# Optimization experiments

Measured on AMD Instinct MI355X. Metric: run time of the kernel, lower is better.

## Reference

```python
import jax, jax.numpy as jnp
import numpy as np

N_NODES = 65536   # entity nodes across batched docs
N_EDGES = 32768   # edges per etype
D_CTX = 768       # PTM hidden size ('n' feature)
D_REL = 97        # relation_num (out_feature)
CHUNK = 1024      # edge chunk for the per-edge bilinear


def setup_inputs() -> dict:
    key = jax.random.key(0)
    ks = jax.random.split(key, 10)
    n = jax.random.normal(ks[0], (N_NODES, D_CTX), jnp.float32)
    e_inter = jax.random.normal(ks[1], (N_EDGES, D_REL), jnp.float32)
    e_intra = jax.random.normal(ks[2], (N_EDGES, D_REL), jnp.float32)
    # nn.Bilinear(768, 97, 1, bias=False): weight [1, 768, 97]
    W_bl = jax.random.normal(ks[3], (1, D_CTX, D_REL), jnp.float32) * 0.02
    # nn.Bilinear(194, 194, 97): weight [97, 194, 194], bias [97]
    W_bl1 = jax.random.normal(ks[4], (D_REL, 2 * D_REL, 2 * D_REL), jnp.float32) * 0.02
    b_bl1 = jnp.zeros((D_REL,), jnp.float32)
    src_inter = jax.random.randint(ks[5], (N_EDGES,), 0, N_NODES, jnp.int32)
    dst_inter = jax.random.randint(ks[6], (N_EDGES,), 0, N_NODES, jnp.int32)
    src_intra = jax.random.randint(ks[7], (N_EDGES,), 0, N_NODES, jnp.int32)
    dst_intra = jax.random.randint(ks[8], (N_EDGES,), 0, N_NODES, jnp.int32)
    return {"n": n, "e_inter": e_inter, "e_intra": e_intra,
            "W_bl": W_bl, "W_bl1": W_bl1, "b_bl1": b_bl1,
            "src_inter": src_inter, "dst_inter": dst_inter,
            "src_intra": src_intra, "dst_intra": dst_intra}


def reference(n, e_inter, e_intra, W_bl, W_bl1, b_bl1,
              src_inter, dst_inter, src_intra, dst_intra):
    num_nodes = n.shape[0]
    # node_reduce: score = bilinear(n[dst], e) -> softmax over incoming edges
    # bl(src_n, e) = n[dst] @ W_bl[0] @ e  (precompute node projection once)
    proj = n @ W_bl[0]                                  # [N, D_REL]

    def node_reduce(e, dst):
        s = jnp.sum(proj[dst] * e, axis=-1)             # per-edge score [E]
        smax = jax.ops.segment_max(s, dst, num_segments=num_nodes)
        ex = jnp.exp(s - smax[dst])
        denom = jax.ops.segment_sum(ex, dst, num_segments=num_nodes)
        alpha = ex / denom[dst]                          # segment softmax
        # attention-weighted sum of mailbox messages -> [N, D_REL]
        return jax.ops.segment_sum(e * alpha[:, None], dst, num_segments=num_nodes)

    # multi_update_all(..., 'stack') over etypes ['inter','intra'] then flatten
    rel = jnp.concatenate([node_reduce(e_inter, dst_inter),
                           node_reduce(e_intra, dst_intra)], axis=-1)  # [N, 194]

    def edge_gate(e, src, dst):
        s_rel = rel[src]                                 # [E, 194]
        d_rel = rel[dst]                                 # [E, 194]
        d_in = s_rel.shape[1]

        def f(args):
            s, d = args                                  # [CHUNK, 194]
            return jnp.einsum('ei,kij,ej->ek', s, W_bl1, d, optimize=True) + b_bl1

        gate = jax.lax.map(f, (s_rel.reshape(-1, CHUNK, d_in),
                               d_rel.reshape(-1, CHUNK, d_in)))
        gate = gate.reshape(e.shape[0], -1)              # [E, D_REL]
        return e + jax.nn.sigmoid(gate) * e

    out_inter = edge_gate(e_inter, src_inter, dst_inter)
    out_intra = edge_gate(e_intra, src_intra, dst_intra)
    return jnp.stack([out_inter, out_intra])             # [2, E, D_REL]
```

## Files before the change

kernel.cpp:

```cpp
#include <hip/hip_runtime.h>
#include <hip/hip_bf16.h>
#include <stdint.h>


typedef __attribute__((ext_vector_type(8))) short short8;
typedef __attribute__((ext_vector_type(4))) float f32x4;
typedef _Float16 half8 __attribute__((ext_vector_type(8)));

#define NN 65536
#define NE1 32768
#define NEG 65536
#define DC 768
#define DR 97
#define DR2 194
#define RELSTR 200
#define KI 194
#define KS 7
#define NT 7
#define EPB 128
#define SSTR 200
#define DSTR 232
#define PSTR 72
#define NDESC_G 2176

#define OFF_REL   0ull
#define OFF_BPK   52428800ull
#define OFF_IDX   62164992ull
#define OFF_SMAX  62427136ull
#define OFF_DEN   62951424ull
#define OFF_META  63475712ull
#define OFF_DESC  63475968ull
#define OFF_WPK   63510784ull

static __device__ __forceinline__ unsigned fkey(float f) {
    unsigned b = __float_as_uint(f);
    return (b & 0x80000000u) ? ~b : (b | 0x80000000u);
}
static __device__ __forceinline__ float funkey(unsigned k) {
    return __uint_as_float((k & 0x80000000u) ? (k & 0x7fffffffu) : ~k);
}
static __device__ __forceinline__ unsigned pk2(_Float16 a, _Float16 b) {
    union { _Float16 h[2]; unsigned u; } x;
    x.h[0] = a; x.h[1] = b;
    return x.u;
}
static __device__ __forceinline__ int nstate(bool zi, bool zx) {
    return zi ? (zx ? 3 : 2) : (zx ? 1 : 0);
}
static __device__ __forceinline__ int nsplit_of(int b) {
    return (b == 0) ? 7 : ((b == 1 || b == 2) ? 4 : 2);
}
static __device__ __forceinline__ int kindbase_of(int b) {
    const int kb[9] = {0, 9, 15, 7, 13, 19, 7, 13, 19};
    return kb[b];
}

__global__ void build_bpk(const float* __restrict__ W, half8* __restrict__ Bpk) {
    int id = blockIdx.x * blockDim.x + threadIdx.x;
    const int total = KI * KS * NT * 64;
    if (id >= total) return;
    int l = id & 63;
    int g = id >> 6;
    int t = g % NT;
    int ks = (g / NT) % KS;
    int i = g / (NT * KS);
    int kk = t * 16 + (l & 15);
    int jb = ks * 32 + (l >> 4) * 8;
    half8 pk;
#pragma unroll
    for (int m = 0; m < 8; ++m) {
        int j = jb + m;
        float f = (kk < DR && j < DR2) ? W[(size_t)kk * (DR2 * DR2) + i * DR2 + j] : 0.f;
        pk[m] = (_Float16)f;
    }
    Bpk[id] = pk;
}

__global__ void build_wpk(const float* __restrict__ Wb, half8* __restrict__ Wpk) {
    int id = blockIdx.x * blockDim.x + threadIdx.x;
    const int total = 24 * NT * 64;
    if (id >= total) return;
    int l = id & 63;
    int g = id >> 6;
    int t = g % NT;
    int k2 = g / NT;
    int col = t * 16 + (l & 15);
    int j0 = k2 * 32 + (l >> 4) * 8;
    half8 pk;
#pragma unroll
    for (int m = 0; m < 8; ++m) {
        float f = (col < DR) ? Wb[(size_t)(j0 + m) * DR + col] : 0.f;
        pk[m] = (_Float16)f;
    }
    Wpk[id] = pk;
}

__launch_bounds__(512, 8)
__global__ void proj_mfma(const float* __restrict__ nmat, const half8* __restrict__ Wpk,
                          float* __restrict__ proj) {
    __shared__ __align__(16) _Float16 a_lds[128][PSTR];
    int tid = threadIdx.x;
    int r0 = blockIdx.x << 7;
    int w = tid >> 6, lane = tid & 63;
    int er = (w << 4) + (lane & 15);
    int lk = lane >> 4;

    f32x4 acc[NT];
#pragma unroll
    for (int t = 0; t < NT; ++t) acc[t] = (f32x4){0.f, 0.f, 0.f, 0.f};

    int srow = tid >> 2;
    int sc0 = (tid & 3) << 4;
    const float* nrow = nmat + (size_t)(r0 + srow) * DC + sc0;

    for (int k0 = 0; k0 < DC; k0 += 64) {
        __syncthreads();
        {
            const f32x4* p = (const f32x4*)(nrow + k0);
            _Float16* dst = &a_lds[srow][sc0];
#pragma unroll
            for (int q = 0; q < 4; ++q) {
                f32x4 v = p[q];
                *(unsigned*)&dst[q * 4]     = pk2((_Float16)v[0], (_Float16)v[1]);
                *(unsigned*)&dst[q * 4 + 2] = pk2((_Float16)v[2], (_Float16)v[3]);
            }
        }
        __syncthreads();
#pragma unroll
        for (int kk = 0; kk < 2; ++kk) {
            half8 af = *(const half8*)&a_lds[er][kk * 32 + lk * 8];
            const half8* bp = Wpk + (size_t)((k0 >> 5) + kk) * (NT * 64) + lane;
#pragma unroll
            for (int t = 0; t < NT; ++t)
                acc[t] = __builtin_amdgcn_mfma_f32_16x16x32_f16(af, bp[t * 64], acc[t], 0, 0, 0);
        }
    }

#pragma unroll
    for (int t = 0; t < NT; ++t) {
        int col = t * 16 + (lane & 15);
        if (col < DR) {
#pragma unroll
            for (int r = 0; r < 4; ++r) {
                int row = r0 + (w << 4) + lk * 4 + r;
                proj[(size_t)row * DR + col] = acc[t][r];
            }
        }
    }
}

__global__ void score_kernel(const float* __restrict__ proj,
                             const float* __restrict__ e_inter, const float* __restrict__ e_intra,
                             const int* __restrict__ dst_inter, const int* __restrict__ dst_intra,
                             float* __restrict__ s_buf, unsigned* __restrict__ smax_key) {
    int wid = (blockIdx.x * blockDim.x + threadIdx.x) >> 6;
    int lane = threadIdx.x & 63;
    if (wid >= NEG) return;
    int et = wid >> 15, le = wid & (NE1 - 1);
    const float* e = (et ? e_intra : e_inter) + (size_t)le * DR;
    int dst = (et ? dst_intra : dst_inter)[le];
    const float* pr = proj + (size_t)dst * DR;
    float p = pr[lane] * e[lane];
    if (lane < DR - 64) p += pr[lane + 64] * e[lane + 64];
#pragma unroll
    for (int off = 32; off > 0; off >>= 1) p += __shfl_down(p, off);
    if (lane == 0) {
        s_buf[wid] = p;
        atomicMax(&smax_key[et * NN + dst], fkey(p));
    }
}

__global__ void accum_kernel(const float* __restrict__ s_buf,
                             const float* __restrict__ e_inter, const float* __restrict__ e_intra,
                             const int* __restrict__ dst_inter, const int* __restrict__ dst_intra,
                             const unsigned* __restrict__ smax_key,
                             float* __restrict__ denom, float* __restrict__ rel) {
    int wid = (blockIdx.x * blockDim.x + threadIdx.x) >> 6;
    int lane = threadIdx.x & 63;
    if (wid >= NEG) return;
    int et = wid >> 15, le = wid & (NE1 - 1);
    const float* e = (et ? e_intra : e_inter) + (size_t)le * DR;
    int dst = (et ? dst_intra : dst_inter)[le];
    float s = s_buf[wid];
    float mx = funkey(smax_key[et * NN + dst]);
    float ex = __expf(s - mx);
    if (lane == 0) atomicAdd(&denom[et * NN + dst], ex);
    float* rrow = rel + (size_t)dst * RELSTR + et * DR;
    atomicAdd(&rrow[lane], e[lane] * ex);
    if (lane < DR - 64) atomicAdd(&rrow[lane + 64], e[lane + 64] * ex);
}

__global__ void dinv_kernel(float* __restrict__ denom) {
    int i = blockIdx.x * blockDim.x + threadIdx.x;
    if (i < 2 * NN) {
        float d = denom[i];
        denom[i] = (d > 0.f) ? (1.f / d) : 0.f;
    }
}

__global__ void classify_kernel(const float* __restrict__ dinv,
                                const int* __restrict__ src_inter, const int* __restrict__ dst_inter,
                                const int* __restrict__ src_intra, const int* __restrict__ dst_intra,
                                unsigned* __restrict__ meta) {
    __shared__ unsigned h[16];
    if (threadIdx.x < 16) h[threadIdx.x] = 0;
    __syncthreads();
    int gid = blockIdx.x * blockDim.x + threadIdx.x;
    if (gid < NEG) {
        int et = gid >> 15, le = gid & (NE1 - 1);
        int sn = (et ? src_intra : src_inter)[le];
        int dn = (et ? dst_intra : dst_inter)[le];
        int ss = nstate(dinv[sn] == 0.f, dinv[NN + sn] == 0.f);
        int ds = nstate(dinv[dn] == 0.f, dinv[NN + dn] == 0.f);
        int b = (ss == 3 || ds == 3) ? 9 : ss * 3 + ds;
        atomicAdd(&h[b], 1u);
    }
    __syncthreads();
    if (threadIdx.x < 10 && h[threadIdx.x])
        atomicAdd(&meta[threadIdx.x], h[threadIdx.x]);
}

__global__ void setup1_kernel(unsigned* __restrict__ meta) {
    if (threadIdx.x != 0 || blockIdx.x != 0) return;
    unsigned run = 0;
    for (int b = 0; b < 10; ++b) {
        meta[32 + b] = run;
        meta[16 + b] = run;
        run += meta[b];
    }
    unsigned c = 0;
    for (int b = 0; b < 9; ++b) {
        meta[52 + b] = c;
        c += ((meta[b] + EPB - 1) / EPB) * (unsigned)nsplit_of(b);
    }
    meta[48] = c;
}

__global__ void setup2_kernel(const unsigned* __restrict__ meta, uint4* __restrict__ desc) {
    int j = blockIdx.x * blockDim.x + threadIdx.x;
    if (j >= (int)meta[48]) return;
    int b = 8;
    for (int q = 1; q < 9; ++q)
        if (j < (int)meta[52 + q]) { b = q - 1; break; }
    int p = j - (int)meta[52 + b];
    int ns = nsplit_of(b);
    int ci = p / ns;
    int si = p - ci * ns;
    int cnt = (int)meta[b];
    int cbase = (int)meta[32 + b] + ci * EPB;
    int ccnt = cnt - ci * EPB;
    if (ccnt > EPB) ccnt = EPB;
    int kind = kindbase_of(b) + si;
    int sclass = b / 3;
    desc[j] = make_uint4((unsigned)kind, (unsigned)cbase, (unsigned)ccnt, (unsigned)sclass);
}

__global__ void scatter_kernel(const float* __restrict__ dinv,
                               const int* __restrict__ src_inter, const int* __restrict__ dst_inter,
                               const int* __restrict__ src_intra, const int* __restrict__ dst_intra,
                               unsigned* __restrict__ meta, int* __restrict__ idxbuf) {
    __shared__ unsigned cur[16];
    __shared__ unsigned base[16];
    if (threadIdx.x < 16) cur[threadIdx.x] = 0;
    __syncthreads();
    int gid = blockIdx.x * blockDim.x + threadIdx.x;
    int b = -1;
    unsigned r = 0;
    if (gid < NEG) {
        int et = gid >> 15, le = gid & (NE1 - 1);
        int sn = (et ? src_intra : src_inter)[le];
        int dn = (et ? dst_intra : dst_inter)[le];
        int ss = nstate(dinv[sn] == 0.f, dinv[NN + sn] == 0.f);
        int ds = nstate(dinv[dn] == 0.f, dinv[NN + dn] == 0.f);
        b = (ss == 3 || ds == 3) ? 9 : ss * 3 + ds;
        r = atomicAdd(&cur[b], 1u);
    }
    __syncthreads();
    if (threadIdx.x < 10 && cur[threadIdx.x])
        base[threadIdx.x] = atomicAdd(&meta[16 + threadIdx.x], cur[threadIdx.x]);
    __syncthreads();
    if (b >= 0) idxbuf[base[b] + r] = gid;
}

__global__ void skip_kernel(const unsigned* __restrict__ meta, const int* __restrict__ idxbuf,
                            const float* __restrict__ e_inter, const float* __restrict__ e_intra,
                            const float* __restrict__ bias, float* __restrict__ out) {
    int n9 = (int)meta[9];
    int base9 = (int)meta[41];
    int k = threadIdx.x;
    float g = 0.f;
    if (k < DR) {
        float b = bias[k];
        g = 1.f + 1.f / (1.f + __expf(-b));
    }
    for (int q = blockIdx.x; q < n9; q += gridDim.x) {
        int gid = idxbuf[base9 + q];
        int et = gid >> 15, le = gid & (NE1 - 1);
        const float* e = (et ? e_intra : e_inter) + (size_t)le * DR;
        if (k < DR) out[(size_t)gid * DR + k] = e[k] * g;
    }
}

#define GATE_BODY(KS0v, KS1v, T0v, T1v)                                        \
    {                                                                          \
        constexpr int NKSv = (KS1v) - (KS0v);                                  \
        constexpr int NTTv = (T1v) - (T0v);                                    \
        f32x4 acc[NTTv];                                                       \
        _Pragma("unroll")                                                      \
        for (int tt = 0; tt < NTTv; ++tt) acc[tt] = (f32x4){0.f, 0.f, 0.f, 0.f}; \
        const half8* bl = Bpk + lane;                                          \
        for (int i = i0; i < iEnd; ++i) {                                      \
            _Float16 sa = buf[er * SSTR + i];                                  \
            half8 sv = {sa, sa, sa, sa, sa, sa, sa, sa};                       \
            const half8* bi = bl + (size_t)((i * KS + (KS0v)) * NT + (T0v)) * 64; \
            _Pragma("unroll")                                                  \
            for (int ks = 0; ks < NKSv; ++ks) {                                \
                half8 af = sv * dv[(KS0v) + ks];                               \
                _Pragma("unroll")                                              \
                for (int tt = 0; tt < NTTv; ++tt) {                            \
                    half8 bv = bi[(ks * NT + tt) * 64];                        \
                    acc[tt] = __builtin_amdgcn_mfma_f32_16x16x32_f16(af, bv, acc[tt], 0, 0, 0); \
                }                                                              \
            }                                                                  \
        }                                                                      \
        _Pragma("unroll")                                                      \
        for (int r = 0; r < 4; ++r) {                                          \
            int row = (w << 4) + lk * 4 + r;                                   \
            if (row < ccnt) {                                                  \
                int gid = idxbuf[cbase + row];                                 \
                int et = gid >> 15, le = gid & (NE1 - 1);                      \
                const float* e = (et ? e_intra : e_inter) + (size_t)le * DR;   \
                float* o = out + (size_t)gid * DR;                             \
                _Pragma("unroll")                                              \
                for (int tt = 0; tt < NTTv; ++tt) {                            \
                    int k = ((T0v) + tt) * 16 + (lane & 15);                   \
                    if (k < DR) {                                              \
                        float g = acc[tt][r] + bias[k];                        \
                        float sg = 1.f / (1.f + __expf(-g));                   \
                        o[k] = e[k] * (1.f + sg);                              \
                    }                                                          \
                }                                                              \
            }                                                                  \
        }                                                                      \
    }

__launch_bounds__(512, 1)
__global__ void gate_all(const float* __restrict__ rel, const float* __restrict__ dinv,
                         const half8* __restrict__ Bpk, const float* __restrict__ bias,
                         const int* __restrict__ src_inter, const int* __restrict__ dst_inter,
                         const int* __restrict__ src_intra, const int* __restrict__ dst_intra,
                         const float* __restrict__ e_inter, const float* __restrict__ e_intra,
                         const int* __restrict__ idxbuf, const unsigned* __restrict__ meta,
                         const uint4* __restrict__ desc, float* __restrict__ out) {
    if (blockIdx.x >= meta[48]) return;
    uint4 de = desc[blockIdx.x];
    int kind = (int)de.x;
    int cbase = (int)de.y;
    int ccnt = (int)de.z;
    int sclass = (int)de.w;
    int i0 = (sclass == 2) ? DR : 0;
    int iEnd = (sclass == 0) ? DR2 : (i0 + DR);

    __shared__ __align__(16) _Float16 buf[EPB * DSTR];
    int tid = threadIdx.x;
    int w = tid >> 6;
    int lane = tid & 63;
    int lk = lane >> 4;
    int er = (w << 4) + (lane & 15);

    if (tid < 256) {
        int edge = tid >> 1;
        int h = tid & 1;
        int rc = cbase + ((edge < ccnt) ? edge : (ccnt - 1));
        int gid = idxbuf[rc];
        int et = gid >> 15, le = gid & (NE1 - 1);
        int dn = (et ? dst_intra : dst_inter)[le];
        float di0 = dinv[dn];
        float di1 = dinv[NN + dn];
        const f32x4* rp = (const f32x4*)(rel + (size_t)dn * RELSTR + h * 100);
        _Float16* row = &buf[edge * DSTR];
#pragma unroll
        for (int q = 0; q < 25; ++q) {
            f32x4 v = rp[q];
            int c = h * 100 + q * 4;
            _Float16 h0 = (_Float16)(v[0] * ((c + 0 < DR) ? di0 : di1));
            _Float16 h1 = (_Float16)(v[1] * ((c + 1 < DR) ? di0 : di1));
            _Float16 h2 = (_Float16)(v[2] * ((c + 2 < DR) ? di0 : di1));
            _Float16 h3 = (_Float16)(v[3] * ((c + 3 < DR) ? di0 : di1));
            *(unsigned*)&row[c] = pk2(h0, h1);
            *(unsigned*)&row[c + 2] = pk2(h2, h3);
        }
        if (h) {
            short8 z = (short8)(short)0;
#pragma unroll
            for (int q = 0; q < 3; ++q)
                *(short8*)&row[200 + q * 8] = z;
        }
    }
    __syncthreads();

    half8 dv[KS];
#pragma unroll
    for (int ks = 0; ks < KS; ++ks)
        dv[ks] = *(const half8*)&buf[er * DSTR + ks * 32 + lk * 8];
    __syncthreads();

    if (tid < 256) {
        int edge = tid >> 1;
        int h = tid & 1;
        int rc = cbase + ((edge < ccnt) ? edge : (ccnt - 1));
        int gid = idxbuf[rc];
        int et = gid >> 15, le = gid & (NE1 - 1);
        int sn = (et ? src_intra : src_inter)[le];
        float di0 = dinv[sn];
        float di1 = dinv[NN + sn];
        const f32x4* rp = (const f32x4*)(rel + (size_t)sn * RELSTR + h * 100);
        _Float16* row = &buf[edge * SSTR];
#pragma unroll
        for (int q = 0; q < 25; ++q) {
            f32x4 v = rp[q];
            int c = h * 100 + q * 4;
            _Float16 h0 = (_Float16)(v[0] * ((c + 0 < DR) ? di0 : di1));
            _Float16 h1 = (_Float16)(v[1] * ((c + 1 < DR) ? di0 : di1));
            _Float16 h2 = (_Float16)(v[2] * ((c + 2 < DR) ? di0 : di1));
            _Float16 h3 = (_Float16)(v[3] * ((c + 3 < DR) ? di0 : di1));
            *(unsigned*)&row[c] = pk2(h0, h1);
            *(unsigned*)&row[c + 2] = pk2(h2, h3);
        }
    }
    __syncthreads();

    switch (kind) {
        case 0:  GATE_BODY(0, 7, 0, 1); break;
        case 1:  GATE_BODY(0, 7, 1, 2); break;
        case 2:  GATE_BODY(0, 7, 2, 3); break;
        case 3:  GATE_BODY(0, 7, 3, 4); break;
        case 4:  GATE_BODY(0, 7, 4, 5); break;
        case 5:  GATE_BODY(0, 7, 5, 6); break;
        case 6:  GATE_BODY(0, 7, 6, 7); break;
        case 7:  GATE_BODY(0, 7, 0, 4); break;
        case 8:  GATE_BODY(0, 7, 4, 7); break;
        case 9:  GATE_BODY(0, 4, 0, 2); break;
        case 10: GATE_BODY(0, 4, 2, 4); break;
        case 11: GATE_BODY(0, 4, 4, 6); break;
        case 12: GATE_BODY(0, 4, 6, 7); break;
        case 13: GATE_BODY(0, 4, 0, 4); break;
        case 14: GATE_BODY(0, 4, 4, 7); break;
        case 15: GATE_BODY(3, 7, 0, 2); break;
        case 16: GATE_BODY(3, 7, 2, 4); break;
        case 17: GATE_BODY(3, 7, 4, 6); break;
        case 18: GATE_BODY(3, 7, 6, 7); break;
        case 19: GATE_BODY(3, 7, 0, 4); break;
        case 20: GATE_BODY(3, 7, 4, 7); break;
        default: break;
    }
}

extern "C" void kernel_launch(void* const* d_in, const int* in_sizes, int n_in,
                              void* d_out, int out_size, void* d_ws, size_t ws_size,
                              hipStream_t stream) {
    (void)in_sizes; (void)n_in; (void)out_size; (void)ws_size;
    const float* nmat     = (const float*)d_in[0];
    const float* e_inter  = (const float*)d_in[1];
    const float* e_intra  = (const float*)d_in[2];
    const float* W_bl     = (const float*)d_in[3];
    const float* W_bl1    = (const float*)d_in[4];
    const float* b_bl1    = (const float*)d_in[5];
    const int* src_inter  = (const int*)d_in[6];
    const int* dst_inter  = (const int*)d_in[7];
    const int* src_intra  = (const int*)d_in[8];
    const int* dst_intra  = (const int*)d_in[9];
    float* out = (float*)d_out;

    char* ws = (char*)d_ws;
    float* regA     = (float*)(ws + OFF_REL);
    half8* Bpk      = (half8*)(ws + OFF_BPK);
    int* idxbuf     = (int*)(ws + OFF_IDX);
    float* s_buf    = (float*)(ws + OFF_IDX);
    unsigned* smax  = (unsigned*)(ws + OFF_SMAX);
    float* denom    = (float*)(ws + OFF_DEN);
    unsigned* meta  = (unsigned*)(ws + OFF_META);
    uint4* desc     = (uint4*)(ws + OFF_DESC);
    half8* Wpk      = (half8*)(ws + OFF_WPK);

    hipMemsetAsync(smax, 0, 524288, stream);
    hipMemsetAsync(denom, 0, 524288, stream);
    hipMemsetAsync(meta, 0, 256, stream);

    build_bpk<<<(KI * KS * NT * 64 + 255) / 256, 256, 0, stream>>>(W_bl1, Bpk);
    build_wpk<<<(24 * NT * 64 + 255) / 256, 256, 0, stream>>>(W_bl, Wpk);
    proj_mfma<<<NN / 128, 512, 0, stream>>>(nmat, Wpk, regA);
    score_kernel<<<NEG / 4, 256, 0, stream>>>(regA, e_inter, e_intra, dst_inter, dst_intra,
                                              s_buf, smax);
    hipMemsetAsync(regA, 0, 52428800, stream);
    accum_kernel<<<NEG / 4, 256, 0, stream>>>(s_buf, e_inter, e_intra, dst_inter, dst_intra,
                                              smax, denom, regA);
    dinv_kernel<<<512, 256, 0, stream>>>(denom);
    classify_kernel<<<NEG / 256, 256, 0, stream>>>(denom, src_inter, dst_inter,
                                                   src_intra, dst_intra, meta);
    setup1_kernel<<<1, 64, 0, stream>>>(meta);
    setup2_kernel<<<(NDESC_G + 255) / 256, 256, 0, stream>>>(meta, desc);
    scatter_kernel<<<NEG / 256, 256, 0, stream>>>(denom, src_inter, dst_inter,
                                                  src_intra, dst_intra, meta, idxbuf);
    skip_kernel<<<2048, 128, 0, stream>>>(meta, idxbuf, e_inter, e_intra, b_bl1, out);
    gate_all<<<NDESC_G, 512, 0, stream>>>(regA, denom, Bpk, b_bl1,
                                          src_inter, dst_inter, src_intra, dst_intra,
                                          e_inter, e_intra, idxbuf, meta, desc, out);
}
```

Before: 644.0 us.

## Process two 16-edge row tiles per wave in gate kernel to reuse B fragments

Each wave in the gate kernel now computes two 16-edge MFMA tiles with separate accumulators, so every B-fragment load from the packed bilinear weight feeds two MFMAs. Blocks shrink from 512 to 256 threads, with launch bounds allowing three blocks per CU. The padded dst buffer stride is replaced by masking the tail K fragment in registers. The aim is to halve global weight traffic per MFMA and raise occupancy, at the cost of roughly doubled accumulator and dv register use.

```diff
diff --git a/kernel.cpp b/kernel.cpp
--- a/kernel.cpp
+++ b/kernel.cpp
@@ -19,7 +19,6 @@
 #define NT 7
 #define EPB 128
 #define SSTR 200
-#define DSTR 232
 #define PSTR 72
 #define NDESC_G 2176
 
@@ -305,27 +304,34 @@
     {                                                                          \
         constexpr int NKSv = (KS1v) - (KS0v);                                  \
         constexpr int NTTv = (T1v) - (T0v);                                    \
-        f32x4 acc[NTTv];                                                       \
+        f32x4 acc0[NTTv], acc1[NTTv];                                          \
         _Pragma("unroll")                                                      \
-        for (int tt = 0; tt < NTTv; ++tt) acc[tt] = (f32x4){0.f, 0.f, 0.f, 0.f}; \
+        for (int tt = 0; tt < NTTv; ++tt) {                                    \
+            acc0[tt] = (f32x4){0.f, 0.f, 0.f, 0.f};                            \
+            acc1[tt] = (f32x4){0.f, 0.f, 0.f, 0.f};                            \
+        }                                                                      \
         const half8* bl = Bpk + lane;                                          \
         for (int i = i0; i < iEnd; ++i) {                                      \
-            _Float16 sa = buf[er * SSTR + i];                                  \
-            half8 sv = {sa, sa, sa, sa, sa, sa, sa, sa};                       \
+            _Float16 s0 = buf[er0 * SSTR + i];                                 \
+            _Float16 s1 = buf[er1 * SSTR + i];                                 \
+            half8 sv0 = {s0, s0, s0, s0, s0, s0, s0, s0};                      \
+            half8 sv1 = {s1, s1, s1, s1, s1, s1, s1, s1};                      \
             const half8* bi = bl + (size_t)((i * KS + (KS0v)) * NT + (T0v)) * 64; \
             _Pragma("unroll")                                                  \
             for (int ks = 0; ks < NKSv; ++ks) {                                \
-                half8 af = sv * dv[(KS0v) + ks];                               \
+                half8 af0 = sv0 * dv0[(KS0v) + ks];                            \
+                half8 af1 = sv1 * dv1[(KS0v) + ks];                            \
                 _Pragma("unroll")                                              \
                 for (int tt = 0; tt < NTTv; ++tt) {                            \
                     half8 bv = bi[(ks * NT + tt) * 64];                        \
-                    acc[tt] = __builtin_amdgcn_mfma_f32_16x16x32_f16(af, bv, acc[tt], 0, 0, 0); \
+                    acc0[tt] = __builtin_amdgcn_mfma_f32_16x16x32_f16(af0, bv, acc0[tt], 0, 0, 0); \
+                    acc1[tt] = __builtin_amdgcn_mfma_f32_16x16x32_f16(af1, bv, acc1[tt], 0, 0, 0); \
                 }                                                              \
             }                                                                  \
         }                                                                      \
         _Pragma("unroll")                                                      \
         for (int r = 0; r < 4; ++r) {                                          \
-            int row = (w << 4) + lk * 4 + r;                                   \
+            int row = (w << 5) + lk * 4 + r;                                   \
             if (row < ccnt) {                                                  \
                 int gid = idxbuf[cbase + row];                                 \
                 int et = gid >> 15, le = gid & (NE1 - 1);                      \
@@ -335,16 +341,35 @@
                 for (int tt = 0; tt < NTTv; ++tt) {                            \
                     int k = ((T0v) + tt) * 16 + (lane & 15);                   \
                     if (k < DR) {                                              \
-                        float g = acc[tt][r] + bias[k];                        \
+                        float g = acc0[tt][r] + bias[k];                       \
                         float sg = 1.f / (1.f + __expf(-g));                   \
                         o[k] = e[k] * (1.f + sg);                              \
                     }                                                          \
                 }                                                              \
             }                                                                  \
         }                                                                      \
-    }
-
-__launch_bounds__(512, 1)
+        _Pragma("unroll")                                                      \
+        for (int r = 0; r < 4; ++r) {                                          \
+            int row = (w << 5) + 16 + lk * 4 + r;                              \
+            if (row < ccnt) {                                                  \
+                int gid = idxbuf[cbase + row];                                 \
+                int et = gid >> 15, le = gid & (NE1 - 1);                      \
+                const float* e = (et ? e_intra : e_inter) + (size_t)le * DR;   \
+                float* o = out + (size_t)gid * DR;                             \
+                _Pragma("unroll")                                              \
+                for (int tt = 0; tt < NTTv; ++tt) {                            \
+                    int k = ((T0v) + tt) * 16 + (lane & 15);                   \
+                    if (k < DR) {                                              \
+                        float g = acc1[tt][r] + bias[k];                       \
+                        float sg = 1.f / (1.f + __expf(-g));                   \
+                        o[k] = e[k] * (1.f + sg);                              \
+                    }                                                          \
+                }                                                              \
+            }                                                                  \
+        }                                                                      \
+    }
+
+__launch_bounds__(256, 3)
 __global__ void gate_all(const float* __restrict__ rel, const float* __restrict__ dinv,
                          const half8* __restrict__ Bpk, const float* __restrict__ bias,
                          const int* __restrict__ src_inter, const int* __restrict__ dst_inter,
@@ -361,14 +386,15 @@
     int i0 = (sclass == 2) ? DR : 0;
     int iEnd = (sclass == 0) ? DR2 : (i0 + DR);
 
-    __shared__ __align__(16) _Float16 buf[EPB * DSTR];
+    __shared__ __align__(16) _Float16 buf[EPB * SSTR];
     int tid = threadIdx.x;
     int w = tid >> 6;
     int lane = tid & 63;
     int lk = lane >> 4;
-    int er = (w << 4) + (lane & 15);
-
-    if (tid < 256) {
+    int er0 = (w << 5) + (lane & 15);
+    int er1 = er0 + 16;
+
+    {
         int edge = tid >> 1;
         int h = tid & 1;
         int rc = cbase + ((edge < ccnt) ? edge : (ccnt - 1));
@@ -378,7 +404,7 @@
         float di0 = dinv[dn];
         float di1 = dinv[NN + dn];
         const f32x4* rp = (const f32x4*)(rel + (size_t)dn * RELSTR + h * 100);
-        _Float16* row = &buf[edge * DSTR];
+        _Float16* row = &buf[edge * SSTR];
 #pragma unroll
         for (int q = 0; q < 25; ++q) {
             f32x4 v = rp[q];
@@ -390,22 +416,23 @@
             *(unsigned*)&row[c] = pk2(h0, h1);
             *(unsigned*)&row[c + 2] = pk2(h2, h3);
         }
-        if (h) {
-            short8 z = (short8)(short)0;
-#pragma unroll
-            for (int q = 0; q < 3; ++q)
-                *(short8*)&row[200 + q * 8] = z;
+    }
+    __syncthreads();
+
+    half8 dv0[KS], dv1[KS];
+#pragma unroll
+    for (int ks = 0; ks < KS; ++ks) {
+        if (ks == 6 && lk > 0) {
+            dv0[ks] = (half8){0, 0, 0, 0, 0, 0, 0, 0};
+            dv1[ks] = (half8){0, 0, 0, 0, 0, 0, 0, 0};
+        } else {
+            dv0[ks] = *(const half8*)&buf[er0 * SSTR + ks * 32 + lk * 8];
+            dv1[ks] = *(const half8*)&buf[er1 * SSTR + ks * 32 + lk * 8];
         }
     }
     __syncthreads();
 
-    half8 dv[KS];
-#pragma unroll
-    for (int ks = 0; ks < KS; ++ks)
-        dv[ks] = *(const half8*)&buf[er * DSTR + ks * 32 + lk * 8];
-    __syncthreads();
-
-    if (tid < 256) {
+    {
         int edge = tid >> 1;
         int h = tid & 1;
         int rc = cbase + ((edge < ccnt) ? edge : (ccnt - 1));
@@ -503,7 +530,7 @@
     scatter_kernel<<<NEG / 256, 256, 0, stream>>>(denom, src_inter, dst_inter,
                                                   src_intra, dst_intra, meta, idxbuf);
     skip_kernel<<<2048, 128, 0, stream>>>(meta, idxbuf, e_inter, e_intra, b_bl1, out);
-    gate_all<<<NDESC_G, 512, 0, stream>>>(regA, denom, Bpk, b_bl1,
+    gate_all<<<NDESC_G, 256, 0, stream>>>(regA, denom, Bpk, b_bl1,
                                           src_inter, dst_inter, src_intra, dst_intra,
                                           e_inter, e_intra, idxbuf, meta, desc, out);
 }
```

Result: slower. 798.5 us (+24.0%).
